# Kernel optimization log

Hardware: AMD Instinct MI355X
Metric: run time of the kernel (lower is better)

Reference implementation:

```python
import jax, jax.numpy as jnp
import numpy as np

L, D_IN, D_OUT, H = 4096, 512, 256, 4
HEAD = D_OUT // H  # 64


def setup_inputs() -> dict:
    key = jax.random.key(0)
    k1, k2, k3, k4, k5 = jax.random.split(key, 5)
    h = jax.random.normal(k1, (L, D_IN), dtype=jnp.float32)
    A = jax.random.randint(k2, (L, L), 0, 2, dtype=jnp.int32)
    W = jax.random.normal(k3, (D_OUT, D_IN), dtype=jnp.float32) * 0.05
    attn = jax.random.normal(k4, (H, 2 * HEAD), dtype=jnp.float32) * 0.05
    out_w = jax.random.normal(k5, (D_OUT, D_OUT), dtype=jnp.float32) * 0.05
    out_b = jnp.zeros((D_OUT,), dtype=jnp.float32)
    return {"h": h, "A": A, "W": W, "attn": attn, "out_w": out_w, "out_b": out_b}


def reference(h, A, W, attn, out_w, out_b):
    # h: (L, D_in), A: (L, L) in {0,1}
    Lq = h.shape[0]
    n_heads, two_d = attn.shape
    d = two_d // 2
    Wh = (h @ W.T).reshape(Lq, n_heads, d)  # (L, H, d)
    # Algebraic rewrite of concat-score: e_ij = a1.Wh_i + a2.Wh_j
    a1, a2 = attn[:, :d], attn[:, d:]
    s_i = jnp.einsum("lhd,hd->lh", Wh, a1)  # (L, H)
    s_j = jnp.einsum("lhd,hd->lh", Wh, a2)  # (L, H)
    e = jax.nn.leaky_relu(s_i[:, None, :] + s_j[None, :, :], negative_slope=0.2)  # (L, L, H)
    mask = (A > 0)[:, :, None]  # (L, L, 1)
    NEG = jnp.asarray(-1e30, e.dtype)
    e = jnp.where(mask, e, NEG)
    # stable masked softmax over j (axis=1); rows with no neighbors -> alpha = 0
    m = jnp.max(e, axis=1, keepdims=True)
    m = jnp.where(m > NEG / 2, m, 0.0)
    ex = jnp.where(mask, jnp.exp(e - m), 0.0)
    denom = jnp.sum(ex, axis=1, keepdims=True)
    alpha = ex / jnp.where(denom > 0, denom, 1.0)  # (L, L, H)
    # dropout is identity in eval mode
    out = jnp.einsum("ijh,jhd->ihd", alpha, Wh).reshape(Lq, n_heads * d)
    return out @ out_w.T + out_b
```

## Files before the change

### kernel.cpp

```cpp
#include <hip/hip_runtime.h>
#include <hip/hip_bf16.h>

#define L_    4096
#define DIN   512
#define DOUT  256
#define NH    4
#define HD    64
#define JW    128

typedef unsigned short u16;
typedef __attribute__((ext_vector_type(8))) short short8;
typedef __attribute__((ext_vector_type(4))) float floatx4;

__device__ __forceinline__ u16 f2bf(float f) {
  union { float f; unsigned u; } v; v.f = f;
  unsigned r = v.u + 0x7fff + ((v.u >> 16) & 1);
  return (u16)(r >> 16);
}
__device__ __forceinline__ unsigned cvt2(float a, float b) {
  __hip_bfloat162 v = __float22bfloat162_rn(make_float2(a, b));
  return *reinterpret_cast<unsigned*>(&v);
}
__device__ __forceinline__ short8 pack8(const float* __restrict__ p) {
  float4 a = *(const float4*)p, b = *(const float4*)(p + 4);
  union { unsigned u[4]; short8 s; } r;
  r.u[0] = cvt2(a.x, a.y); r.u[1] = cvt2(a.z, a.w);
  r.u[2] = cvt2(b.x, b.y); r.u[3] = cvt2(b.z, b.w);
  return r.s;
}

__device__ __forceinline__ void mfma_cdmap(int lane, int* rowm, int* colm) {
  const int c0 = lane & 15;
  union { u16 u[8]; short8 s; } a1, b1, a2, b2;
  const u16 one = f2bf(1.f), cid = f2bf((float)c0);
  #pragma unroll
  for (int j = 0; j < 8; ++j) { a1.u[j] = cid; b1.u[j] = one; a2.u[j] = one; b2.u[j] = cid; }
  floatx4 z = {0.f, 0.f, 0.f, 0.f};
  floatx4 dr = __builtin_amdgcn_mfma_f32_16x16x32_bf16(a1.s, b1.s, z, 0, 0, 0);
  floatx4 dc = __builtin_amdgcn_mfma_f32_16x16x32_bf16(a2.s, b2.s, z, 0, 0, 0);
  #pragma unroll
  for (int r = 0; r < 4; ++r) {
    rowm[r] = (int)(dr[r] * 0.03125f + 0.5f);
    colm[r] = (int)(dc[r] * 0.03125f + 0.5f);
  }
}

__global__ __launch_bounds__(256) void k_ab(const int* __restrict__ A,
                                            unsigned* __restrict__ Abits,
                                            const float* __restrict__ W,
                                            u16* __restrict__ Wf) {
  const int t = threadIdx.x;
  const int g = blockIdx.x * 256 + t;
  const int lane = t & 63;
  #pragma unroll
  for (int r = 0; r < 8; ++r) {
    const size_t gi = (size_t)r * 524288 + g;
    int4 v = *(const int4*)(A + gi * 4);
    unsigned nib = (v.x > 0 ? 1u : 0u) | (v.y > 0 ? 2u : 0u)
                 | (v.z > 0 ? 4u : 0u) | (v.w > 0 ? 8u : 0u);
    unsigned part = nib << ((lane & 7) * 4);
    part |= __shfl_xor(part, 1, 64);
    part |= __shfl_xor(part, 2, 64);
    part |= __shfl_xor(part, 4, 64);
    if ((lane & 7) == 0) Abits[gi >> 3] = part;
  }
  if (blockIdx.x < 16) {
    const int col = g >> 4, kblock = g & 15;
    const int cg = col >> 6, nt = (col >> 4) & 3, c0 = col & 15;
    const float* src = W + (size_t)col * DIN + kblock * 32;
    u16* dst = Wf + ((size_t)(cg * 4 + nt) * 16 + kblock) * 512 + c0 * 8;
    #pragma unroll
    for (int q = 0; q < 4; ++q) {
      short8 v = pack8(src + q * 8);
      *(short8*)(dst + q * 128) = v;
    }
  }
}

__global__ __launch_bounds__(256) void k1_wh(
    const float* __restrict__ h, const u16* __restrict__ Wf,
    const float* __restrict__ attn,
    u16* __restrict__ WhTf, float* __restrict__ s1g, float2* __restrict__ bdg)
{
  const int bid = blockIdx.x;
  const int tile = bid >> 2, cg = bid & 3;
  const int i0 = tile * 16;
  const int t = threadIdx.x;
  const int wv = t >> 6, lane = t & 63, q = lane >> 4, c0 = lane & 15;
  const int nt = wv;
  int rowm[4], colm[4];
  mfma_cdmap(lane, rowm, colm);

  __shared__ u16  hT[16][DIN + 8];
  __shared__ float pS[16][HD + 4];

  #pragma unroll
  for (int rep = 0; rep < 4; ++rep) {
    const int idx = rep * 256 + t;
    const int row = idx >> 6, c8 = (idx & 63) * 8;
    const float* hp = h + (size_t)(i0 + row) * DIN + c8;
    float4 a = *(const float4*)hp;
    float4 b = *(const float4*)(hp + 4);
    union { unsigned u[4]; int4 v; } pk;
    pk.u[0] = cvt2(a.x, a.y); pk.u[1] = cvt2(a.z, a.w);
    pk.u[2] = cvt2(b.x, b.y); pk.u[3] = cvt2(b.z, b.w);
    *(int4*)&hT[row][c8] = pk.v;
  }
  __syncthreads();

  floatx4 acc = {0.f, 0.f, 0.f, 0.f};
  #pragma unroll
  for (int ks = 0; ks < 16; ++ks) {
    const int kb = ks * 32 + q * 8;
    short8 af = *(const short8*)&hT[c0][kb];
    short8 bf = *(const short8*)(Wf + ((size_t)(cg * 4 + nt) * 16 + ks) * 512 + lane * 8);
    acc = __builtin_amdgcn_mfma_f32_16x16x32_bf16(af, bf, acc, 0, 0, 0);
  }
  #pragma unroll
  for (int r = 0; r < 4; ++r)
    pS[rowm[r]][nt * 16 + colm[r]] = acc[r];
  __syncthreads();

  if (wv == 0) {
    const int r = lane & 15, qt = lane >> 4;
    float s1 = 0.f, s2 = 0.f;
    #pragma unroll
    for (int dd = 0; dd < 16; ++dd) {
      const int d = qt * 16 + dd;
      float v = pS[r][d];
      s1 += v * attn[cg * 128 + d];
      s2 += v * attn[cg * 128 + 64 + d];
    }
    s1 += __shfl_xor(s1, 16, 64); s1 += __shfl_xor(s1, 32, 64);
    s2 += __shfl_xor(s2, 16, 64); s2 += __shfl_xor(s2, 32, 64);
    if (lane < 16) {
      s1g[cg * L_ + i0 + r] = s1;
      bdg[cg * L_ + i0 + r] = make_float2(__expf(s2), __expf(0.2f * s2));
    }
  }
  if (wv == 1) {
    const int dl = t - 64;
    const int nt2 = dl >> 4, dc0 = dl & 15;
    const int jblock = i0 >> 5, qbase = (i0 & 31) >> 3;
    u16* base = WhTf + ((size_t)(cg * 4 + nt2) * JW + jblock) * 512 + dc0 * 8;
    #pragma unroll
    for (int jh = 0; jh < 2; ++jh) {
      const int i = jh * 8;
      union { unsigned u[4]; int4 v; } pk;
      pk.u[0] = cvt2(pS[i + 0][dl], pS[i + 1][dl]);
      pk.u[1] = cvt2(pS[i + 2][dl], pS[i + 3][dl]);
      pk.u[2] = cvt2(pS[i + 4][dl], pS[i + 5][dl]);
      pk.u[3] = cvt2(pS[i + 6][dl], pS[i + 7][dl]);
      *(int4*)(base + (qbase + jh) * 128) = pk.v;
    }
  }
}

__global__ __launch_bounds__(1024) void k2_attn(
    const unsigned* __restrict__ Abits, const u16* __restrict__ WhTf,
    const float* __restrict__ s1g, const float2* __restrict__ bdg,
    const float* __restrict__ out_w, const float* __restrict__ out_b,
    float* __restrict__ out)
{
  const int i0 = blockIdx.x * 16;
  const int t = threadIdx.x;
  const int wv = t >> 6, lane = t & 63, q = lane >> 4, c0 = lane & 15;
  const int hd = wv & 3, jc = wv >> 2;

  __shared__ float pA[NH][16][HD + 4];
  __shared__ float pB[NH][16][HD + 4];
  __shared__ float dden[NH][4][16];
  __shared__ float rcpS[NH][16];
  __shared__ u16  CnL[16][DOUT + 8];
  __shared__ unsigned AbitL[16][JW + 2];

  {
    const int row = t >> 6, l = t & 63;
    uint2 w2 = *(const uint2*)&Abits[(size_t)(i0 + row) * JW + l * 2];
    AbitL[row][l * 2] = w2.x;
    AbitL[row][l * 2 + 1] = w2.y;
  }
  int rowm[4], colm[4];
  mfma_cdmap(lane, rowm, colm);
  __syncthreads();

  const float s1v = s1g[hd * L_ + i0 + c0];
  const float av = __expf(s1v);
  const float cv = __expf(0.2f * s1v);
  const float th = __expf(-s1v);
  const float2* bdh = bdg + (size_t)hd * L_;
  const u16* Wc = WhTf + (size_t)(hd * 4) * JW * 512 + (size_t)(jc * 32) * 512 + lane * 8;
  const int jbase = jc * 1024;

  floatx4 acc[4] = {};
  float dpart = 0.f;

  union PF { unsigned u[4]; short8 s; };

  auto issueV = [&](int kt, float4* v) {
    const float2* p = bdh + jbase + kt * 32 + q * 8;
    v[0] = *(const float4*)p;       v[1] = *(const float4*)(p + 2);
    v[2] = *(const float4*)(p + 4); v[3] = *(const float4*)(p + 6);
  };
  auto issueW = [&](int kt, short8* w) {
    #pragma unroll
    for (int nt = 0; nt < 4; ++nt)
      w[nt] = *(const short8*)(Wc + ((size_t)nt * JW + kt) * 512);
  };
  auto sm8 = [&](const float4* v, int kt, PF& pf) {
    const unsigned mb = (AbitL[c0][jc * 32 + kt] >> (q * 8)) & 0xffu;
    const float bb[8] = {v[0].x, v[0].z, v[1].x, v[1].z, v[2].x, v[2].z, v[3].x, v[3].z};
    const float dd[8] = {v[0].y, v[0].w, v[1].y, v[1].w, v[2].y, v[2].w, v[3].y, v[3].w};
    float ex[8];
    #pragma unroll
    for (int jj = 0; jj < 8; ++jj) {
      float p = (bb[jj] >= th) ? (av * bb[jj]) : (cv * dd[jj]);
      ex[jj] = ((mb >> jj) & 1u) ? p : 0.f;
      dpart += ex[jj];
    }
    pf.u[0] = cvt2(ex[0], ex[1]); pf.u[1] = cvt2(ex[2], ex[3]);
    pf.u[2] = cvt2(ex[4], ex[5]); pf.u[3] = cvt2(ex[6], ex[7]);
  };
  auto mfma4 = [&](PF& pf, const short8* w) {
    #pragma unroll
    for (int nt = 0; nt < 4; ++nt)
      acc[nt] = __builtin_amdgcn_mfma_f32_16x16x32_bf16(pf.s, w[nt], acc[nt], 0, 0, 0);
  };

  float4 vA[4], vB[4];
  short8 wA[4], wB[4];
  PF pfA, pfB;

  issueV(0, vA); issueW(0, wA);
  issueV(1, vB); issueW(1, wB);
  __builtin_amdgcn_sched_barrier(0);
  sm8(vA, 0, pfA);

  #pragma unroll 1
  for (int u = 0; u < 15; ++u) {
    const int kt = 2 * u;
    issueV(kt + 2, vA);
    __builtin_amdgcn_sched_barrier(0);
    sm8(vB, kt + 1, pfB);
    mfma4(pfA, wA);
    __builtin_amdgcn_sched_barrier(0);
    issueW(kt + 2, wA);
    issueV(kt + 3, vB);
    __builtin_amdgcn_sched_barrier(0);
    mfma4(pfB, wB);
    __builtin_amdgcn_sched_barrier(0);
    issueW(kt + 3, wB);
    sm8(vA, kt + 2, pfA);
    __builtin_amdgcn_sched_barrier(0);
  }
  mfma4(pfA, wA);
  sm8(vB, 31, pfB);
  mfma4(pfB, wB);

  dpart += __shfl_xor(dpart, 16, 64);
  dpart += __shfl_xor(dpart, 32, 64);
  if (lane < 16) dden[hd][jc][lane] = dpart;

  auto writeT = [&](float (*P)[HD + 4]) {
    #pragma unroll
    for (int nt = 0; nt < 4; ++nt)
      #pragma unroll
      for (int r = 0; r < 4; ++r)
        P[rowm[r]][nt * 16 + colm[r]] = acc[nt][r];
  };
  auto addB2A = [&]() {
    const int h2 = t >> 8, rem = t & 255, row = rem >> 4, d4 = (rem & 15) * 4;
    float4* a = (float4*)&pA[h2][row][d4];
    float4 bv = *(float4*)&pB[h2][row][d4];
    float4 av2 = *a;
    av2.x += bv.x; av2.y += bv.y; av2.z += bv.z; av2.w += bv.w;
    *a = av2;
  };

  if (jc == 0) writeT(pA[hd]);
  if (jc == 1) writeT(pB[hd]);
  __syncthreads();
  if (t < 64) {
    const int hh = t >> 4, r = t & 15;
    float den = dden[hh][0][r] + dden[hh][1][r] + dden[hh][2][r] + dden[hh][3][r];
    rcpS[hh][r] = (den > 0.f) ? (1.f / den) : 0.f;
  }
  addB2A();
  __syncthreads();
  if (jc == 2) writeT(pB[hd]);
  __syncthreads();
  addB2A();
  __syncthreads();
  if (jc == 3) writeT(pB[hd]);
  __syncthreads();
  addB2A();
  __syncthreads();

  {
    const int row = t >> 6, c4 = (t & 63) * 4;
    #pragma unroll
    for (int x = 0; x < 4; ++x) {
      const int col = c4 + x;
      const int hh = col >> 6, d = col & 63;
      CnL[row][col] = f2bf(pA[hh][row][d] * rcpS[hh][row]);
    }
  }
  __syncthreads();

  if (wv < 4) {
    const int cg = wv;
    floatx4 o[4] = {};
    #pragma unroll
    for (int kt = 0; kt < DOUT / 32; ++kt) {
      const int kb2 = kt * 32 + q * 8;
      short8 afr = *(const short8*)(&CnL[c0][kb2]);
      #pragma unroll
      for (int nt = 0; nt < 4; ++nt) {
        const int col = cg * 64 + nt * 16 + c0;
        short8 bfo = pack8(out_w + (size_t)col * DOUT + kb2);
        o[nt] = __builtin_amdgcn_mfma_f32_16x16x32_bf16(afr, bfo, o[nt], 0, 0, 0);
      }
    }
    #pragma unroll
    for (int nt = 0; nt < 4; ++nt)
      #pragma unroll
      for (int r = 0; r < 4; ++r) {
        const int col = cg * 64 + nt * 16 + colm[r];
        out[(size_t)(i0 + rowm[r]) * DOUT + col] = o[nt][r] + out_b[col];
      }
  }
}

extern "C" void kernel_launch(void* const* d_in, const int* in_sizes, int n_in,
                              void* d_out, int out_size, void* d_ws, size_t ws_size,
                              hipStream_t stream) {
  const float* h     = (const float*)d_in[0];
  const int*   A     = (const int*)d_in[1];
  const float* W     = (const float*)d_in[2];
  const float* attn  = (const float*)d_in[3];
  const float* out_w = (const float*)d_in[4];
  const float* out_b = (const float*)d_in[5];
  float* outp = (float*)d_out;

  const size_t WHTF_B  = (size_t)DOUT * L_ * 2;
  const size_t S1_B    = (size_t)NH * L_ * 4;
  const size_t BD_B    = (size_t)NH * L_ * 8;
  const size_t ABITS_B = (size_t)L_ * JW * 4;
  const size_t AB_OFF  = WHTF_B + S1_B + BD_B;

  u16*    WhTf = (u16*)d_ws;
  float*  s1g  = (float*)((char*)d_ws + WHTF_B);
  float2* bdg  = (float2*)((char*)d_ws + WHTF_B + S1_B);
  unsigned* Abits = (ws_size >= AB_OFF + ABITS_B)
                  ? (unsigned*)((char*)d_ws + AB_OFF)
                  : (unsigned*)((char*)d_out + 2097152);
  u16* Wf = (u16*)d_out;

  hipLaunchKernelGGL(k_ab, dim3(2048), dim3(256), 0, stream, A, Abits, W, Wf);
  hipLaunchKernelGGL(k1_wh, dim3(L_ / 16 * 4), dim3(256), 0, stream,
                     h, Wf, attn, WhTf, s1g, bdg);
  hipLaunchKernelGGL(k2_attn, dim3(L_ / 16), dim3(1024), 0, stream,
                     Abits, WhTf, s1g, bdg, out_w, out_b, outp);
}
```

Before: 155.1 us.

## Stage Wh tiles through LDS with async global_load_lds double buffering

The attention kernel's main loop now fetches Wh B-operand tiles asynchronously into double-buffered LDS using global_load_lds, replacing the register-prefetch software pipeline. Each iteration loads from the current LDS buffer while prefetching the next, and it waits on vmcnt explicitly. Shared memory moves to one dynamic allocation of about 136 KB, with the epilogue buffers aliased onto the staging area after a barrier. The aim is to cut register pressure and global-load latency stalls. The cost is much larger LDS use per block and reliance on hand-tuned waitcnt ordering, where the bdg loads share vmcnt with the async copies.

After: 158.0 us. About the same (+1.9%).

```diff
diff --git a/kernel.cpp b/kernel.cpp
--- a/kernel.cpp
+++ b/kernel.cpp
@@ -12,6 +12,9 @@
 typedef __attribute__((ext_vector_type(8))) short short8;
 typedef __attribute__((ext_vector_type(4))) float floatx4;
 
+#define VMWAIT(n) asm volatile("s_waitcnt vmcnt(" #n ")" ::: "memory")
+#define SB() __builtin_amdgcn_sched_barrier(0)
+
 __device__ __forceinline__ u16 f2bf(float f) {
   union { float f; unsigned u; } v; v.f = f;
   unsigned r = v.u + 0x7fff + ((v.u >> 16) & 1);
@@ -27,6 +30,11 @@
   r.u[0] = cvt2(a.x, a.y); r.u[1] = cvt2(a.z, a.w);
   r.u[2] = cvt2(b.x, b.y); r.u[3] = cvt2(b.z, b.w);
   return r.s;
+}
+__device__ __forceinline__ void gll16(const u16* g, u16* l) {
+  __builtin_amdgcn_global_load_lds(
+      (__attribute__((address_space(1))) void*)g,
+      (__attribute__((address_space(3))) void*)l, 16, 0, 0);
 }
 
 __device__ __forceinline__ void mfma_cdmap(int lane, int* rowm, int* colm) {
@@ -156,23 +164,24 @@
   }
 }
 
+#define STG_U16_BUF   32768
+#define ABIT_OFF      131072
+#define DYN_LDS_BYTES 139392
+
 __global__ __launch_bounds__(1024) void k2_attn(
     const unsigned* __restrict__ Abits, const u16* __restrict__ WhTf,
     const float* __restrict__ s1g, const float2* __restrict__ bdg,
     const float* __restrict__ out_w, const float* __restrict__ out_b,
     float* __restrict__ out)
 {
+  extern __shared__ char dynLds[];
+  u16* stgW = (u16*)dynLds;
+  unsigned (*AbitL)[130] = (unsigned(*)[130])(dynLds + ABIT_OFF);
+
   const int i0 = blockIdx.x * 16;
   const int t = threadIdx.x;
   const int wv = t >> 6, lane = t & 63, q = lane >> 4, c0 = lane & 15;
   const int hd = wv & 3, jc = wv >> 2;
-
-  __shared__ float pA[NH][16][HD + 4];
-  __shared__ float pB[NH][16][HD + 4];
-  __shared__ float dden[NH][4][16];
-  __shared__ float rcpS[NH][16];
-  __shared__ u16  CnL[16][DOUT + 8];
-  __shared__ unsigned AbitL[16][JW + 2];
 
   {
     const int row = t >> 6, l = t & 63;
@@ -188,77 +197,79 @@
   const float av = __expf(s1v);
   const float cv = __expf(0.2f * s1v);
   const float th = __expf(-s1v);
-  const float2* bdh = bdg + (size_t)hd * L_;
+  const float2* bdh = bdg + (size_t)hd * L_ + jc * 1024;
   const u16* Wc = WhTf + (size_t)(hd * 4) * JW * 512 + (size_t)(jc * 32) * 512 + lane * 8;
-  const int jbase = jc * 1024;
+
+  u16* stg0 = stgW + (size_t)wv * 2048;
+  u16* stg1 = stgW + STG_U16_BUF + (size_t)wv * 2048;
 
   floatx4 acc[4] = {};
   float dpart = 0.f;
-
   union PF { unsigned u[4]; short8 s; };
 
-  auto issueV = [&](int kt, float4* v) {
-    const float2* p = bdh + jbase + kt * 32 + q * 8;
-    v[0] = *(const float4*)p;       v[1] = *(const float4*)(p + 2);
-    v[2] = *(const float4*)(p + 4); v[3] = *(const float4*)(p + 6);
-  };
-  auto issueW = [&](int kt, short8* w) {
-    #pragma unroll
-    for (int nt = 0; nt < 4; ++nt)
-      w[nt] = *(const short8*)(Wc + ((size_t)nt * JW + kt) * 512);
-  };
-  auto sm8 = [&](const float4* v, int kt, PF& pf) {
+  #pragma unroll
+  for (int nt = 0; nt < 4; ++nt)
+    gll16(Wc + (size_t)nt * JW * 512, stg0 + nt * 512);
+
+  #pragma unroll 1
+  for (int kt = 0; kt < 32; ++kt) {
+    u16* cur = (kt & 1) ? stg1 : stg0;
+    u16* nxt = (kt & 1) ? stg0 : stg1;
+    const float2* p = bdh + kt * 32 + q * 8;
+    float4 v0 = *(const float4*)p;
+    float4 v1 = *(const float4*)(p + 2);
+    float4 v2 = *(const float4*)(p + 4);
+    float4 v3 = *(const float4*)(p + 6);
+    VMWAIT(4); SB();
+    short8 w0 = *(const short8*)(cur + 0 * 512 + lane * 8);
+    short8 w1 = *(const short8*)(cur + 1 * 512 + lane * 8);
+    short8 w2 = *(const short8*)(cur + 2 * 512 + lane * 8);
+    short8 w3 = *(const short8*)(cur + 3 * 512 + lane * 8);
+    if (kt < 31) {
+      const u16* src = Wc + (size_t)(kt + 1) * 512;
+      #pragma unroll
+      for (int nt = 0; nt < 4; ++nt)
+        gll16(src + (size_t)nt * JW * 512, nxt + nt * 512);
+    }
+    SB();
     const unsigned mb = (AbitL[c0][jc * 32 + kt] >> (q * 8)) & 0xffu;
-    const float bb[8] = {v[0].x, v[0].z, v[1].x, v[1].z, v[2].x, v[2].z, v[3].x, v[3].z};
-    const float dd[8] = {v[0].y, v[0].w, v[1].y, v[1].w, v[2].y, v[2].w, v[3].y, v[3].w};
-    float ex[8];
-    #pragma unroll
-    for (int jj = 0; jj < 8; ++jj) {
-      float p = (bb[jj] >= th) ? (av * bb[jj]) : (cv * dd[jj]);
-      ex[jj] = ((mb >> jj) & 1u) ? p : 0.f;
-      dpart += ex[jj];
-    }
-    pf.u[0] = cvt2(ex[0], ex[1]); pf.u[1] = cvt2(ex[2], ex[3]);
-    pf.u[2] = cvt2(ex[4], ex[5]); pf.u[3] = cvt2(ex[6], ex[7]);
-  };
-  auto mfma4 = [&](PF& pf, const short8* w) {
-    #pragma unroll
-    for (int nt = 0; nt < 4; ++nt)
-      acc[nt] = __builtin_amdgcn_mfma_f32_16x16x32_bf16(pf.s, w[nt], acc[nt], 0, 0, 0);
-  };
-
-  float4 vA[4], vB[4];
-  short8 wA[4], wB[4];
-  PF pfA, pfB;
-
-  issueV(0, vA); issueW(0, wA);
-  issueV(1, vB); issueW(1, wB);
-  __builtin_amdgcn_sched_barrier(0);
-  sm8(vA, 0, pfA);
-
-  #pragma unroll 1
-  for (int u = 0; u < 15; ++u) {
-    const int kt = 2 * u;
-    issueV(kt + 2, vA);
-    __builtin_amdgcn_sched_barrier(0);
-    sm8(vB, kt + 1, pfB);
-    mfma4(pfA, wA);
-    __builtin_amdgcn_sched_barrier(0);
-    issueW(kt + 2, wA);
-    issueV(kt + 3, vB);
-    __builtin_amdgcn_sched_barrier(0);
-    mfma4(pfB, wB);
-    __builtin_amdgcn_sched_barrier(0);
-    issueW(kt + 3, wB);
-    sm8(vA, kt + 2, pfA);
-    __builtin_amdgcn_sched_barrier(0);
-  }
-  mfma4(pfA, wA);
-  sm8(vB, 31, pfB);
-  mfma4(pfB, wB);
+    float e0 = (v0.x >= th) ? (av * v0.x) : (cv * v0.y);
+    float e1 = (v0.z >= th) ? (av * v0.z) : (cv * v0.w);
+    float e2 = (v1.x >= th) ? (av * v1.x) : (cv * v1.y);
+    float e3 = (v1.z >= th) ? (av * v1.z) : (cv * v1.w);
+    float e4 = (v2.x >= th) ? (av * v2.x) : (cv * v2.y);
+    float e5 = (v2.z >= th) ? (av * v2.z) : (cv * v2.w);
+    float e6 = (v3.x >= th) ? (av * v3.x) : (cv * v3.y);
+    float e7 = (v3.z >= th) ? (av * v3.z) : (cv * v3.w);
+    e0 = (mb & 1u)   ? e0 : 0.f;
+    e1 = (mb & 2u)   ? e1 : 0.f;
+    e2 = (mb & 4u)   ? e2 : 0.f;
+    e3 = (mb & 8u)   ? e3 : 0.f;
+    e4 = (mb & 16u)  ? e4 : 0.f;
+    e5 = (mb & 32u)  ? e5 : 0.f;
+    e6 = (mb & 64u)  ? e6 : 0.f;
+    e7 = (mb & 128u) ? e7 : 0.f;
+    dpart += ((e0 + e1) + (e2 + e3)) + ((e4 + e5) + (e6 + e7));
+    PF pf;
+    pf.u[0] = cvt2(e0, e1); pf.u[1] = cvt2(e2, e3);
+    pf.u[2] = cvt2(e4, e5); pf.u[3] = cvt2(e6, e7);
+    acc[0] = __builtin_amdgcn_mfma_f32_16x16x32_bf16(pf.s, w0, acc[0], 0, 0, 0);
+    acc[1] = __builtin_amdgcn_mfma_f32_16x16x32_bf16(pf.s, w1, acc[1], 0, 0, 0);
+    acc[2] = __builtin_amdgcn_mfma_f32_16x16x32_bf16(pf.s, w2, acc[2], 0, 0, 0);
+    acc[3] = __builtin_amdgcn_mfma_f32_16x16x32_bf16(pf.s, w3, acc[3], 0, 0, 0);
+  }
 
   dpart += __shfl_xor(dpart, 16, 64);
   dpart += __shfl_xor(dpart, 32, 64);
+
+  __syncthreads();
+
+  float (*pA)[16][HD + 4]  = (float(*)[16][HD + 4])(dynLds);
+  float (*pB)[16][HD + 4]  = (float(*)[16][HD + 4])(dynLds + 17408);
+  float (*dden)[4][16]     = (float(*)[4][16])(dynLds + 34816);
+  float (*rcpS)[16]        = (float(*)[16])(dynLds + 35840);
+  u16  (*CnL)[DOUT + 8]    = (u16(*)[DOUT + 8])(dynLds + 36096);
+
   if (lane < 16) dden[hd][jc][lane] = dpart;
 
   auto writeT = [&](float (*P)[HD + 4]) {
@@ -356,9 +367,17 @@
                   : (unsigned*)((char*)d_out + 2097152);
   u16* Wf = (u16*)d_out;
 
+  static bool attr_set = false;
+  if (!attr_set) {
+    hipFuncSetAttribute(reinterpret_cast<const void*>(k2_attn),
+                        hipFuncAttributeMaxDynamicSharedMemorySize,
+                        DYN_LDS_BYTES);
+    attr_set = true;
+  }
+
   hipLaunchKernelGGL(k_ab, dim3(2048), dim3(256), 0, stream, A, Abits, W, Wf);
   hipLaunchKernelGGL(k1_wh, dim3(L_ / 16 * 4), dim3(256), 0, stream,
                      h, Wf, attn, WhTf, s1g, bdg);
-  hipLaunchKernelGGL(k2_attn, dim3(L_ / 16), dim3(1024), 0, stream,
+  hipLaunchKernelGGL(k2_attn, dim3(L_ / 16), dim3(1024), DYN_LDS_BYTES, stream,
                      Abits, WhTf, s1g, bdg, out_w, out_b, outp);
 }
```

## Split attention kernel per head across blocks and combine outputs with atomics

Applied to the files above, without the earlier changes.

The attention kernel now launches one 512-thread block per (row tile, head) pair instead of one 1024-thread block covering all four heads. Each block splits the neighbour range across 8 waves and reduces their partials in shared memory in a shorter sequence with fewer barriers. Each block then projects its head's slice through out_w and accumulates into the output with atomicAdd, which requires zeroing the output first with a memset. This gives 4x more, smaller blocks for occupancy and load balance, at the cost of atomic traffic, an extra memset and a workspace layout that no longer falls back to d_out when the workspace is small.

New measurement: 166.1 us. 1.07x slower.

```diff
diff --git a/kernel.cpp b/kernel.cpp
--- a/kernel.cpp
+++ b/kernel.cpp
@@ -156,29 +156,32 @@
   }
 }
 
-__global__ __launch_bounds__(1024) void k2_attn(
+__global__ __launch_bounds__(512) void k2_attn(
     const unsigned* __restrict__ Abits, const u16* __restrict__ WhTf,
     const float* __restrict__ s1g, const float2* __restrict__ bdg,
     const float* __restrict__ out_w, const float* __restrict__ out_b,
     float* __restrict__ out)
 {
-  const int i0 = blockIdx.x * 16;
+  const int bid = blockIdx.x;
+  const int tile = bid >> 2, hd = bid & 3;
+  const int i0 = tile * 16;
   const int t = threadIdx.x;
   const int wv = t >> 6, lane = t & 63, q = lane >> 4, c0 = lane & 15;
-  const int hd = wv & 3, jc = wv >> 2;
-
-  __shared__ float pA[NH][16][HD + 4];
-  __shared__ float pB[NH][16][HD + 4];
-  __shared__ float dden[NH][4][16];
-  __shared__ float rcpS[NH][16];
-  __shared__ u16  CnL[16][DOUT + 8];
+  const int jc = wv;
+
+  __shared__ float pP[4][16][HD + 4];
+  __shared__ float dden[8][16];
+  __shared__ float rcpS[16];
+  __shared__ u16  CnL[16][HD + 8];
   __shared__ unsigned AbitL[16][JW + 2];
 
   {
-    const int row = t >> 6, l = t & 63;
-    uint2 w2 = *(const uint2*)&Abits[(size_t)(i0 + row) * JW + l * 2];
-    AbitL[row][l * 2] = w2.x;
-    AbitL[row][l * 2 + 1] = w2.y;
+    const int row = t >> 5, l = t & 31;
+    uint4 w4 = *(const uint4*)&Abits[(size_t)(i0 + row) * JW + l * 4];
+    AbitL[row][l * 4 + 0] = w4.x;
+    AbitL[row][l * 4 + 1] = w4.y;
+    AbitL[row][l * 4 + 2] = w4.z;
+    AbitL[row][l * 4 + 3] = w4.w;
   }
   int rowm[4], colm[4];
   mfma_cdmap(lane, rowm, colm);
@@ -189,12 +192,11 @@
   const float cv = __expf(0.2f * s1v);
   const float th = __expf(-s1v);
   const float2* bdh = bdg + (size_t)hd * L_;
-  const u16* Wc = WhTf + (size_t)(hd * 4) * JW * 512 + (size_t)(jc * 32) * 512 + lane * 8;
-  const int jbase = jc * 1024;
+  const u16* Wc = WhTf + (size_t)(hd * 4) * JW * 512 + (size_t)(jc * 16) * 512 + lane * 8;
+  const int jbase = jc * 512;
 
   floatx4 acc[4] = {};
   float dpart = 0.f;
-
   union PF { unsigned u[4]; short8 s; };
 
   auto issueV = [&](int kt, float4* v) {
@@ -208,7 +210,7 @@
       w[nt] = *(const short8*)(Wc + ((size_t)nt * JW + kt) * 512);
   };
   auto sm8 = [&](const float4* v, int kt, PF& pf) {
-    const unsigned mb = (AbitL[c0][jc * 32 + kt] >> (q * 8)) & 0xffu;
+    const unsigned mb = (AbitL[c0][jc * 16 + kt] >> (q * 8)) & 0xffu;
     const float bb[8] = {v[0].x, v[0].z, v[1].x, v[1].z, v[2].x, v[2].z, v[3].x, v[3].z};
     const float dd[8] = {v[0].y, v[0].w, v[1].y, v[1].w, v[2].y, v[2].w, v[3].y, v[3].w};
     float ex[8];
@@ -237,7 +239,7 @@
   sm8(vA, 0, pfA);
 
   #pragma unroll 1
-  for (int u = 0; u < 15; ++u) {
+  for (int u = 0; u < 7; ++u) {
     const int kt = 2 * u;
     issueV(kt + 2, vA);
     __builtin_amdgcn_sched_barrier(0);
@@ -254,56 +256,52 @@
     __builtin_amdgcn_sched_barrier(0);
   }
   mfma4(pfA, wA);
-  sm8(vB, 31, pfB);
+  sm8(vB, 15, pfB);
   mfma4(pfB, wB);
 
   dpart += __shfl_xor(dpart, 16, 64);
   dpart += __shfl_xor(dpart, 32, 64);
-  if (lane < 16) dden[hd][jc][lane] = dpart;
-
-  auto writeT = [&](float (*P)[HD + 4]) {
+  if (lane < 16) dden[jc][lane] = dpart;
+
+  if (jc < 4) {
     #pragma unroll
     for (int nt = 0; nt < 4; ++nt)
       #pragma unroll
       for (int r = 0; r < 4; ++r)
-        P[rowm[r]][nt * 16 + colm[r]] = acc[nt][r];
-  };
-  auto addB2A = [&]() {
-    const int h2 = t >> 8, rem = t & 255, row = rem >> 4, d4 = (rem & 15) * 4;
-    float4* a = (float4*)&pA[h2][row][d4];
-    float4 bv = *(float4*)&pB[h2][row][d4];
-    float4 av2 = *a;
-    av2.x += bv.x; av2.y += bv.y; av2.z += bv.z; av2.w += bv.w;
+        pP[jc][rowm[r]][nt * 16 + colm[r]] = acc[nt][r];
+  }
+  __syncthreads();
+  if (jc >= 4) {
+    #pragma unroll
+    for (int nt = 0; nt < 4; ++nt)
+      #pragma unroll
+      for (int r = 0; r < 4; ++r)
+        pP[jc - 4][rowm[r]][nt * 16 + colm[r]] += acc[nt][r];
+  }
+  __syncthreads();
+  {
+    const int e = t * 2, row = e >> 6, d = e & 63;
+    float2* a = (float2*)&pP[0][row][d];
+    float2 x1 = *(const float2*)&pP[1][row][d];
+    float2 x2 = *(const float2*)&pP[2][row][d];
+    float2 x3 = *(const float2*)&pP[3][row][d];
+    float2 av2 = *a;
+    av2.x += x1.x + x2.x + x3.x;
+    av2.y += x1.y + x2.y + x3.y;
     *a = av2;
-  };
-
-  if (jc == 0) writeT(pA[hd]);
-  if (jc == 1) writeT(pB[hd]);
-  __syncthreads();
-  if (t < 64) {
-    const int hh = t >> 4, r = t & 15;
-    float den = dden[hh][0][r] + dden[hh][1][r] + dden[hh][2][r] + dden[hh][3][r];
-    rcpS[hh][r] = (den > 0.f) ? (1.f / den) : 0.f;
-  }
-  addB2A();
-  __syncthreads();
-  if (jc == 2) writeT(pB[hd]);
-  __syncthreads();
-  addB2A();
-  __syncthreads();
-  if (jc == 3) writeT(pB[hd]);
-  __syncthreads();
-  addB2A();
+  }
+  if (t < 16) {
+    float den = 0.f;
+    #pragma unroll
+    for (int j = 0; j < 8; ++j) den += dden[j][t];
+    rcpS[t] = (den > 0.f) ? (1.f / den) : 0.f;
+  }
   __syncthreads();
 
   {
-    const int row = t >> 6, c4 = (t & 63) * 4;
-    #pragma unroll
-    for (int x = 0; x < 4; ++x) {
-      const int col = c4 + x;
-      const int hh = col >> 6, d = col & 63;
-      CnL[row][col] = f2bf(pA[hh][row][d] * rcpS[hh][row]);
-    }
+    const int e = t * 2, row = e >> 6, d = e & 63;
+    CnL[row][d]     = f2bf(pP[0][row][d]     * rcpS[row]);
+    CnL[row][d + 1] = f2bf(pP[0][row][d + 1] * rcpS[row]);
   }
   __syncthreads();
 
@@ -311,13 +309,13 @@
     const int cg = wv;
     floatx4 o[4] = {};
     #pragma unroll
-    for (int kt = 0; kt < DOUT / 32; ++kt) {
-      const int kb2 = kt * 32 + q * 8;
+    for (int kt2 = 0; kt2 < 2; ++kt2) {
+      const int kb2 = kt2 * 32 + q * 8;
       short8 afr = *(const short8*)(&CnL[c0][kb2]);
       #pragma unroll
       for (int nt = 0; nt < 4; ++nt) {
         const int col = cg * 64 + nt * 16 + c0;
-        short8 bfo = pack8(out_w + (size_t)col * DOUT + kb2);
+        short8 bfo = pack8(out_w + (size_t)col * DOUT + hd * 64 + kb2);
         o[nt] = __builtin_amdgcn_mfma_f32_16x16x32_bf16(afr, bfo, o[nt], 0, 0, 0);
       }
     }
@@ -326,7 +324,8 @@
       #pragma unroll
       for (int r = 0; r < 4; ++r) {
         const int col = cg * 64 + nt * 16 + colm[r];
-        out[(size_t)(i0 + rowm[r]) * DOUT + col] = o[nt][r] + out_b[col];
+        float add = o[nt][r] + (hd == 0 ? out_b[col] : 0.f);
+        atomicAdd(&out[(size_t)(i0 + rowm[r]) * DOUT + col], add);
       }
   }
 }
@@ -347,18 +346,19 @@
   const size_t BD_B    = (size_t)NH * L_ * 8;
   const size_t ABITS_B = (size_t)L_ * JW * 4;
   const size_t AB_OFF  = WHTF_B + S1_B + BD_B;
-
-  u16*    WhTf = (u16*)d_ws;
-  float*  s1g  = (float*)((char*)d_ws + WHTF_B);
-  float2* bdg  = (float2*)((char*)d_ws + WHTF_B + S1_B);
-  unsigned* Abits = (ws_size >= AB_OFF + ABITS_B)
-                  ? (unsigned*)((char*)d_ws + AB_OFF)
-                  : (unsigned*)((char*)d_out + 2097152);
-  u16* Wf = (u16*)d_out;
+  const size_t WF_OFF  = AB_OFF + ABITS_B;
+
+  u16*      WhTf  = (u16*)d_ws;
+  float*    s1g   = (float*)((char*)d_ws + WHTF_B);
+  float2*   bdg   = (float2*)((char*)d_ws + WHTF_B + S1_B);
+  unsigned* Abits = (unsigned*)((char*)d_ws + AB_OFF);
+  u16*      Wf    = (u16*)((char*)d_ws + WF_OFF);
+
+  hipMemsetAsync(outp, 0, (size_t)L_ * DOUT * sizeof(float), stream);
 
   hipLaunchKernelGGL(k_ab, dim3(2048), dim3(256), 0, stream, A, Abits, W, Wf);
   hipLaunchKernelGGL(k1_wh, dim3(L_ / 16 * 4), dim3(256), 0, stream,
                      h, Wf, attn, WhTf, s1g, bdg);
-  hipLaunchKernelGGL(k2_attn, dim3(L_ / 16), dim3(1024), 0, stream,
+  hipLaunchKernelGGL(k2_attn, dim3(L_ / 16 * 4), dim3(512), 0, stream,
                      Abits, WhTf, s1g, bdg, out_w, out_b, outp);
 }
```
